# Kernel tuning notes

Measured on AMD Instinct MI355X. Metric: run time of the kernel, lower is better.

The kernel has to match this reference:

```python
import jax, jax.numpy as jnp
import numpy as np

N_NODES = 100000
N_EDGES = 400000
MB = 9          # minimal_basis_size
REP = 45        # equi-rep dim per 9x9 block
OUT = 32        # irreps_out dim ('32x0e')
HID = 64        # hidden layer of FullyConnectedNet


def _voigt(c):
    """Diagonal followed by strict upper triangle of a square [..., n, n] block."""
    n = c.shape[-1]
    diag = jnp.diagonal(c, axis1=-2, axis2=-1)
    iu, ju = np.triu_indices(n, 1)
    off = c[..., iu, ju]
    return jnp.concatenate([diag, off], axis=-1)


def generate_equi_rep(m):
    """[..., 9, 9] -> [..., 45]: s/p/d diagonal blocks in voigt form + flattened off-diagonal blocks."""
    s = m[..., 0:1, 0:1]
    p = m[..., 1:4, 1:4]
    d = m[..., 4:, 4:]
    sp = m[..., 0:1, 1:4]
    sd = m[..., 0:1, 4:]
    pd = m[..., 1:4, 4:]
    flat = lambda t: t.reshape(t.shape[:-2] + (-1,))
    return jnp.concatenate(
        [_voigt(s), _voigt(p), _voigt(d), flat(sp), flat(sd), flat(pd)], axis=-1
    )


def setup_inputs() -> dict:
    key = jax.random.key(0)
    k = jax.random.split(key, 6)
    return {
        "f_nodes": jax.random.normal(k[0], (N_NODES, 2 * MB * MB), dtype=jnp.float32),
        "f_edges": jax.random.normal(k[1], (N_EDGES, 2 * MB * MB), dtype=jnp.float32),
        "edge_index": jax.random.randint(k[2], (2, N_EDGES), 0, N_NODES),
        "W_tp": jax.random.normal(k[3], (REP, REP, OUT), dtype=jnp.float32),
        "W_fc1": jax.random.normal(k[4], (OUT, HID), dtype=jnp.float32),
        "W_fc2": jax.random.normal(k[5], (HID, REP), dtype=jnp.float32),
    }


def reference(f_nodes, f_edges, edge_index, W_tp, W_fc1, W_fc2):
    row = edge_index[0]
    # node / edge 9x9 blocks -> 45-d equivariant reps, 2 channels each
    fn = generate_equi_rep(f_nodes.reshape(-1, 2, MB, MB))  # [N, 2, 45]
    fe = generate_equi_rep(f_edges.reshape(-1, 2, MB, MB))  # [E, 2, 45]
    fn = fn[row]                                            # gather -> [E, 2, 45]
    # FullyConnectedTensorProduct on scalar irreps == normalized bilinear form
    tp = jnp.einsum("eci,ecj,ijk->eck", fn, fe, W_tp) / jnp.sqrt(jnp.float32(REP * REP))
    # e3nn FullyConnectedNet([OUT, HID, REP]) with default act=None: normalized linears
    h = (tp @ W_fc1) / jnp.sqrt(jnp.float32(OUT))
    out = (h @ W_fc2) / jnp.sqrt(jnp.float32(HID))
    return out  # [E, 2, 45]
```

## Files before the change

### kernel.cpp

```cpp
#include <hip/hip_runtime.h>
#include <math.h>

#define N_NODES_ 100000
#define N_EDGES_ 400000
#define NPB 8
#define THREADS 512

__constant__ int REP_OFF_C[45] = {
  0,
  10, 20, 30,
  11, 12, 21,
  40, 50, 60, 70, 80,
  41, 42, 43, 44, 51, 52, 53, 61, 62, 71,
  1, 2, 3,
  4, 5, 6, 7, 8,
  13, 14, 15, 16, 17, 22, 23, 24, 25, 26, 31, 32, 33, 34, 35
};

__global__ void zero_u32_k(unsigned* p, int n) {
  int i = blockIdx.x * blockDim.x + threadIdx.x;
  if (i < n) p[i] = 0u;
}

__global__ void hist_k(const int* __restrict__ row, unsigned* __restrict__ deg, int n) {
  int i = blockIdx.x * blockDim.x + threadIdx.x;
  if (i < n) atomicAdd(&deg[row[i]], 1u);
}

__global__ __launch_bounds__(1024)
void scan_k(const unsigned* __restrict__ deg, unsigned* __restrict__ row_ptr,
            unsigned* __restrict__ cursor, unsigned n) {
  __shared__ unsigned wsum[16];
  __shared__ unsigned carry_s;
  const int tid = threadIdx.x;
  const int lane = tid & 63;
  const int w = tid >> 6;
  if (tid == 0) carry_s = 0u;
  __syncthreads();
  const unsigned CH = 1024u * 8u;
  for (unsigned base = 0; base < n; base += CH) {
    unsigned v[8]; unsigned s = 0;
    #pragma unroll
    for (int q = 0; q < 8; ++q) {
      unsigned i = base + (unsigned)tid * 8u + q;
      v[q] = (i < n) ? deg[i] : 0u;
      s += v[q];
    }
    unsigned incl = s;
    #pragma unroll
    for (int off = 1; off < 64; off <<= 1) {
      unsigned t2 = __shfl_up(incl, off);
      if (lane >= off) incl += t2;
    }
    if (lane == 63) wsum[w] = incl;
    __syncthreads();
    if (tid == 0) {
      unsigned a = 0;
      #pragma unroll
      for (int i2 = 0; i2 < 16; ++i2) { unsigned t3 = wsum[i2]; wsum[i2] = a; a += t3; }
    }
    __syncthreads();
    unsigned run = carry_s + wsum[w] + (incl - s);
    #pragma unroll
    for (int q = 0; q < 8; ++q) {
      unsigned i = base + (unsigned)tid * 8u + q;
      if (i < n) { row_ptr[i] = run; cursor[i] = run; }
      run += v[q];
    }
    __syncthreads();
    if (tid == 1023) carry_s = run;
    __syncthreads();
  }
  if (tid == 0) row_ptr[n] = carry_s;
}

__global__ void scatter_k(const int* __restrict__ row, unsigned* __restrict__ cursor,
                          unsigned* __restrict__ edge_list, int n) {
  int i = blockIdx.x * blockDim.x + threadIdx.x;
  if (i < n) {
    unsigned p = atomicAdd(&cursor[row[i]], 1u);
    edge_list[p] = (unsigned)i;
  }
}

__global__ void wc_k(const float* __restrict__ fc1, const float* __restrict__ fc2,
                     float* __restrict__ Wc) {
  int idx = blockIdx.x * blockDim.x + threadIdx.x;
  if (idx < 32 * 45) {
    int k = idx / 45, r = idx - k * 45;
    float s = 0.f;
    #pragma unroll
    for (int h = 0; h < 64; ++h) s += fc1[k * 64 + h] * fc2[h * 45 + r];
    const float SCALE = 1.0f / (45.0f * 8.0f * sqrtf(32.0f));
    Wc[idx] = s * SCALE;
  }
}

__global__ __launch_bounds__(THREADS)
void fused_k(const float* __restrict__ f_nodes, const float* __restrict__ f_edges,
             const float* __restrict__ W_tp, const float* __restrict__ Wc,
             const unsigned* __restrict__ row_ptr, const unsigned* __restrict__ edge_list,
             float* __restrict__ out) {
  __shared__ float A_lds[16 * 1440];
  __shared__ float fn_lds[45][16];
  __shared__ float ferep_lds[8][2][48];
  __shared__ float tp_lds[8][2][32];
  __shared__ unsigned tasks[512];
  __shared__ int t_count;

  const int tid = threadIdx.x;
  const int node_base = blockIdx.x * NPB;

  if (tid == 0) t_count = 0;
  for (int idx = tid; idx < NPB * 2 * 45; idx += THREADS) {
    int ln = idx / 90; int rem = idx - ln * 90; int c = rem / 45; int j = rem - c * 45;
    int node = node_base + ln;
    fn_lds[j][ln * 2 + c] = f_nodes[(size_t)node * 162 + c * 81 + REP_OFF_C[j]];
  }
  __syncthreads();

  if (tid < NPB) {
    int n = node_base + tid;
    unsigned s = row_ptr[n], e = row_ptr[n + 1];
    for (unsigned q = s; q < e; ++q) {
      unsigned eid = edge_list[q];
      int pos = atomicAdd(&t_count, 2);
      if (pos + 1 < 512) {
        unsigned b = (eid << 4) | ((unsigned)tid << 1);
        tasks[pos] = b;
        tasks[pos + 1] = b | 1u;
      }
    }
  }

  float acc0[16], acc1[16], acc2[16];
  #pragma unroll
  for (int nc = 0; nc < 16; ++nc) { acc0[nc] = 0.f; acc1[nc] = 0.f; acc2[nc] = 0.f; }
  const int jk0 = tid, jk1 = tid + THREADS, jk2 = tid + 2 * THREADS;
  const bool v2 = (jk2 < 1440);
  for (int i = 0; i < 45; ++i) {
    float fv[16];
    #pragma unroll
    for (int q = 0; q < 4; ++q)
      *(float4*)&fv[q * 4] = *(const float4*)&fn_lds[i][q * 4];
    const float* wrow = W_tp + i * 1440;
    float w0 = wrow[jk0];
    float w1 = wrow[jk1];
    float w2 = v2 ? wrow[jk2] : 0.f;
    #pragma unroll
    for (int nc = 0; nc < 16; ++nc) {
      acc0[nc] = fmaf(w0, fv[nc], acc0[nc]);
      acc1[nc] = fmaf(w1, fv[nc], acc1[nc]);
      acc2[nc] = fmaf(w2, fv[nc], acc2[nc]);
    }
  }
  #pragma unroll
  for (int nc = 0; nc < 16; ++nc) {
    A_lds[nc * 1440 + jk0] = acc0[nc];
    A_lds[nc * 1440 + jk1] = acc1[nc];
    if (v2) A_lds[nc * 1440 + jk2] = acc2[nc];
  }
  __syncthreads();

  const int wid = tid >> 6, lane = tid & 63;
  const int th = lane >> 5, k = lane & 31;
  float wc1[32], wc2[32];
  #pragma unroll
  for (int k2 = 0; k2 < 32; ++k2) {
    wc1[k2] = Wc[k2 * 45 + k];
    wc2[k2] = (k < 13) ? Wc[k2 * 45 + k + 32] : 0.f;
  }
  const int T = t_count;
  for (int p2 = wid * 2; p2 < T; p2 += 16) {
    const int idx = p2 + th;
    const bool valid = idx < T;
    const unsigned task = tasks[valid ? idx : 0];
    const int e = (int)(task >> 4);
    const int nc = (int)(task & 15u);
    const int c = (int)(task & 1u);
    const float* fe = f_edges + (size_t)e * 162 + c * 81;
    ferep_lds[wid][th][k] = fe[REP_OFF_C[k]];
    if (k < 13) ferep_lds[wid][th][k + 32] = fe[REP_OFF_C[k + 32]];
    asm volatile("s_waitcnt lgkmcnt(0)" ::: "memory");
    float acc = 0.f;
    const float* Arow = &A_lds[nc * 1440 + k];
    const float* fr = &ferep_lds[wid][th][0];
    #pragma unroll
    for (int j = 0; j < 45; ++j)
      acc = fmaf(fr[j], Arow[j * 32], acc);
    tp_lds[wid][th][k] = acc;
    asm volatile("s_waitcnt lgkmcnt(0)" ::: "memory");
    const float* tpp = &tp_lds[wid][th][0];
    float o1 = 0.f, o2 = 0.f;
    #pragma unroll
    for (int k2 = 0; k2 < 32; ++k2) {
      float tv = tpp[k2];
      o1 = fmaf(tv, wc1[k2], o1);
      o2 = fmaf(tv, wc2[k2], o2);
    }
    if (valid) {
      float* op = out + (size_t)e * 90 + c * 45;
      op[k] = o1;
      if (k < 13) op[k + 32] = o2;
    }
  }
}

extern "C" void kernel_launch(void* const* d_in, const int* in_sizes, int n_in,
                              void* d_out, int out_size, void* d_ws, size_t ws_size,
                              hipStream_t stream) {
  const float* f_nodes = (const float*)d_in[0];
  const float* f_edges = (const float*)d_in[1];
  const int* edge_index = (const int*)d_in[2];
  const float* W_tp = (const float*)d_in[3];
  const float* W_fc1 = (const float*)d_in[4];
  const float* W_fc2 = (const float*)d_in[5];
  float* out = (float*)d_out;

  char* ws = (char*)d_ws;
  unsigned* deg_cursor = (unsigned*)ws;
  unsigned* row_ptr   = (unsigned*)(ws + 400000);
  unsigned* edge_list = (unsigned*)(ws + 800016);
  float*    Wc        = (float*)(ws + 800016 + 1600000);

  const int* row = edge_index;

  zero_u32_k<<<(N_NODES_ + 255) / 256, 256, 0, stream>>>(deg_cursor, N_NODES_);
  wc_k<<<6, 256, 0, stream>>>(W_fc1, W_fc2, Wc);
  hist_k<<<(N_EDGES_ + 255) / 256, 256, 0, stream>>>(row, deg_cursor, N_EDGES_);
  scan_k<<<1, 1024, 0, stream>>>(deg_cursor, row_ptr, deg_cursor, N_NODES_);
  scatter_k<<<(N_EDGES_ + 255) / 256, 256, 0, stream>>>(row, deg_cursor, edge_list, N_EDGES_);
  fused_k<<<N_NODES_ / NPB, THREADS, 0, stream>>>(f_nodes, f_edges, W_tp, Wc,
                                                  row_ptr, edge_list, out);
}
```

Measured before the change: 1.655 ms.

## Assign one wavefront per node and hold its contracted weights in registers

Blocks shrink to 4 nodes and 256 threads with a 3-block occupancy hint, which halves the per-block LDS for the node-contracted W_tp slab. Each wavefront now owns one node: its 32 lanes per channel load their 45 A values into registers once, then walk the node's edge list straight from the CSR. Edge features are read directly from global memory instead of being staged in LDS, and the shared task queue with its atomics is removed. The 32->45 projection is done by 45 lanes per channel, and the zero kernel becomes a memset. The trade-off is poorer balance, since a wave's work follows its node's degree, plus higher register pressure from the 45-entry A array.

```diff
diff --git a/kernel.cpp b/kernel.cpp
--- a/kernel.cpp
+++ b/kernel.cpp
@@ -3,9 +3,19 @@
 
 #define N_NODES_ 100000
 #define N_EDGES_ 400000
-#define NPB 8
-#define THREADS 512
-
+#define NPB 4
+#define THREADS 256
+
+constexpr int REP_OFF[45] = {
+  0,
+  10, 20, 30,
+  11, 12, 21,
+  40, 50, 60, 70, 80,
+  41, 42, 43, 44, 51, 52, 53, 61, 62, 71,
+  1, 2, 3,
+  4, 5, 6, 7, 8,
+  13, 14, 15, 16, 17, 22, 23, 24, 25, 26, 31, 32, 33, 34, 35
+};
 __constant__ int REP_OFF_C[45] = {
   0,
   10, 20, 30,
@@ -16,11 +26,6 @@
   4, 5, 6, 7, 8,
   13, 14, 15, 16, 17, 22, 23, 24, 25, 26, 31, 32, 33, 34, 35
 };
-
-__global__ void zero_u32_k(unsigned* p, int n) {
-  int i = blockIdx.x * blockDim.x + threadIdx.x;
-  if (i < n) p[i] = 0u;
-}
 
 __global__ void hist_k(const int* __restrict__ row, unsigned* __restrict__ deg, int n) {
   int i = blockIdx.x * blockDim.x + threadIdx.x;
@@ -96,112 +101,96 @@
   }
 }
 
-__global__ __launch_bounds__(THREADS)
+__global__ __launch_bounds__(THREADS, 3)
 void fused_k(const float* __restrict__ f_nodes, const float* __restrict__ f_edges,
              const float* __restrict__ W_tp, const float* __restrict__ Wc,
              const unsigned* __restrict__ row_ptr, const unsigned* __restrict__ edge_list,
              float* __restrict__ out) {
-  __shared__ float A_lds[16 * 1440];
-  __shared__ float fn_lds[45][16];
-  __shared__ float ferep_lds[8][2][48];
-  __shared__ float tp_lds[8][2][32];
-  __shared__ unsigned tasks[512];
-  __shared__ int t_count;
+  __shared__ float A_lds[8 * 1440];
+  __shared__ float fn_lds[45][8];
+  __shared__ float tp_lds[4][64];
 
   const int tid = threadIdx.x;
   const int node_base = blockIdx.x * NPB;
 
-  if (tid == 0) t_count = 0;
   for (int idx = tid; idx < NPB * 2 * 45; idx += THREADS) {
-    int ln = idx / 90; int rem = idx - ln * 90; int c = rem / 45; int j = rem - c * 45;
-    int node = node_base + ln;
-    fn_lds[j][ln * 2 + c] = f_nodes[(size_t)node * 162 + c * 81 + REP_OFF_C[j]];
+    int ncl = idx / 45; int j = idx - ncl * 45;
+    int ln = ncl >> 1, c = ncl & 1;
+    fn_lds[j][ncl] = f_nodes[(size_t)(node_base + ln) * 162 + c * 81 + REP_OFF_C[j]];
   }
   __syncthreads();
 
-  if (tid < NPB) {
-    int n = node_base + tid;
-    unsigned s = row_ptr[n], e = row_ptr[n + 1];
-    for (unsigned q = s; q < e; ++q) {
-      unsigned eid = edge_list[q];
-      int pos = atomicAdd(&t_count, 2);
-      if (pos + 1 < 512) {
-        unsigned b = (eid << 4) | ((unsigned)tid << 1);
-        tasks[pos] = b;
-        tasks[pos + 1] = b | 1u;
+  float accA[8][6];
+  #pragma unroll
+  for (int nc = 0; nc < 8; ++nc)
+    #pragma unroll
+    for (int q = 0; q < 6; ++q) accA[nc][q] = 0.f;
+
+  for (int i = 0; i < 45; ++i) {
+    float fv[8];
+    *(float4*)&fv[0] = *(const float4*)&fn_lds[i][0];
+    *(float4*)&fv[4] = *(const float4*)&fn_lds[i][4];
+    const float* wrow = W_tp + i * 1440;
+    #pragma unroll
+    for (int q = 0; q < 6; ++q) {
+      const int jk = tid + q * THREADS;
+      float w = (jk < 1440) ? wrow[jk] : 0.f;
+      #pragma unroll
+      for (int nc = 0; nc < 8; ++nc)
+        accA[nc][q] = fmaf(w, fv[nc], accA[nc][q]);
+    }
+  }
+  #pragma unroll
+  for (int q = 0; q < 6; ++q) {
+    const int jk = tid + q * THREADS;
+    if (jk < 1440) {
+      #pragma unroll
+      for (int nc = 0; nc < 8; ++nc) A_lds[nc * 1440 + jk] = accA[nc][q];
+    }
+  }
+  __syncthreads();
+
+  const int wv = tid >> 6, lane = tid & 63;
+  const int th = lane >> 5, k = lane & 31;
+
+  float wcr[32];
+  {
+    const int r = (lane < 45) ? lane : 0;
+    #pragma unroll
+    for (int k2 = 0; k2 < 32; ++k2) wcr[k2] = Wc[k2 * 45 + r];
+  }
+
+  float Areg[45];
+  {
+    const float* Ab = &A_lds[(wv * 2 + th) * 1440 + k];
+    #pragma unroll
+    for (int j = 0; j < 45; ++j) Areg[j] = Ab[j * 32];
+  }
+
+  const int n = node_base + wv;
+  const unsigned s = row_ptr[n], e = row_ptr[n + 1];
+  for (unsigned q = s; q < e; ++q) {
+    const unsigned eid = edge_list[q];
+    const float* fe = f_edges + (size_t)eid * 162 + th * 81;
+    float acc = 0.f;
+    #pragma unroll
+    for (int j = 0; j < 45; ++j)
+      acc = fmaf(fe[REP_OFF[j]], Areg[j], acc);
+    tp_lds[wv][lane] = acc;
+    asm volatile("s_waitcnt lgkmcnt(0)" ::: "memory");
+    #pragma unroll
+    for (int c = 0; c < 2; ++c) {
+      const float* tb = &tp_lds[wv][c * 32];
+      float o = 0.f;
+      #pragma unroll
+      for (int q2 = 0; q2 < 8; ++q2) {
+        float4 t4 = *(const float4*)&tb[q2 * 4];
+        o = fmaf(t4.x, wcr[q2 * 4 + 0], o);
+        o = fmaf(t4.y, wcr[q2 * 4 + 1], o);
+        o = fmaf(t4.z, wcr[q2 * 4 + 2], o);
+        o = fmaf(t4.w, wcr[q2 * 4 + 3], o);
       }
-    }
-  }
-
-  float acc0[16], acc1[16], acc2[16];
-  #pragma unroll
-  for (int nc = 0; nc < 16; ++nc) { acc0[nc] = 0.f; acc1[nc] = 0.f; acc2[nc] = 0.f; }
-  const int jk0 = tid, jk1 = tid + THREADS, jk2 = tid + 2 * THREADS;
-  const bool v2 = (jk2 < 1440);
-  for (int i = 0; i < 45; ++i) {
-    float fv[16];
-    #pragma unroll
-    for (int q = 0; q < 4; ++q)
-      *(float4*)&fv[q * 4] = *(const float4*)&fn_lds[i][q * 4];
-    const float* wrow = W_tp + i * 1440;
-    float w0 = wrow[jk0];
-    float w1 = wrow[jk1];
-    float w2 = v2 ? wrow[jk2] : 0.f;
-    #pragma unroll
-    for (int nc = 0; nc < 16; ++nc) {
-      acc0[nc] = fmaf(w0, fv[nc], acc0[nc]);
-      acc1[nc] = fmaf(w1, fv[nc], acc1[nc]);
-      acc2[nc] = fmaf(w2, fv[nc], acc2[nc]);
-    }
-  }
-  #pragma unroll
-  for (int nc = 0; nc < 16; ++nc) {
-    A_lds[nc * 1440 + jk0] = acc0[nc];
-    A_lds[nc * 1440 + jk1] = acc1[nc];
-    if (v2) A_lds[nc * 1440 + jk2] = acc2[nc];
-  }
-  __syncthreads();
-
-  const int wid = tid >> 6, lane = tid & 63;
-  const int th = lane >> 5, k = lane & 31;
-  float wc1[32], wc2[32];
-  #pragma unroll
-  for (int k2 = 0; k2 < 32; ++k2) {
-    wc1[k2] = Wc[k2 * 45 + k];
-    wc2[k2] = (k < 13) ? Wc[k2 * 45 + k + 32] : 0.f;
-  }
-  const int T = t_count;
-  for (int p2 = wid * 2; p2 < T; p2 += 16) {
-    const int idx = p2 + th;
-    const bool valid = idx < T;
-    const unsigned task = tasks[valid ? idx : 0];
-    const int e = (int)(task >> 4);
-    const int nc = (int)(task & 15u);
-    const int c = (int)(task & 1u);
-    const float* fe = f_edges + (size_t)e * 162 + c * 81;
-    ferep_lds[wid][th][k] = fe[REP_OFF_C[k]];
-    if (k < 13) ferep_lds[wid][th][k + 32] = fe[REP_OFF_C[k + 32]];
-    asm volatile("s_waitcnt lgkmcnt(0)" ::: "memory");
-    float acc = 0.f;
-    const float* Arow = &A_lds[nc * 1440 + k];
-    const float* fr = &ferep_lds[wid][th][0];
-    #pragma unroll
-    for (int j = 0; j < 45; ++j)
-      acc = fmaf(fr[j], Arow[j * 32], acc);
-    tp_lds[wid][th][k] = acc;
-    asm volatile("s_waitcnt lgkmcnt(0)" ::: "memory");
-    const float* tpp = &tp_lds[wid][th][0];
-    float o1 = 0.f, o2 = 0.f;
-    #pragma unroll
-    for (int k2 = 0; k2 < 32; ++k2) {
-      float tv = tpp[k2];
-      o1 = fmaf(tv, wc1[k2], o1);
-      o2 = fmaf(tv, wc2[k2], o2);
-    }
-    if (valid) {
-      float* op = out + (size_t)e * 90 + c * 45;
-      op[k] = o1;
-      if (k < 13) op[k + 32] = o2;
+      if (lane < 45) out[(size_t)eid * 90 + c * 45 + lane] = o;
     }
   }
 }
@@ -225,7 +214,7 @@
 
   const int* row = edge_index;
 
-  zero_u32_k<<<(N_NODES_ + 255) / 256, 256, 0, stream>>>(deg_cursor, N_NODES_);
+  hipMemsetAsync(deg_cursor, 0, (size_t)N_NODES_ * 4, stream);
   wc_k<<<6, 256, 0, stream>>>(W_fc1, W_fc2, Wc);
   hist_k<<<(N_EDGES_ + 255) / 256, 256, 0, stream>>>(row, deg_cursor, N_EDGES_);
   scan_k<<<1, 1024, 0, stream>>>(deg_cursor, row_ptr, deg_cursor, N_NODES_);
```

Measured after the change: 1.564 ms. 5.5% less time.
